# Kernel optimization log

Hardware: AMD Instinct MI355X
Metric: run time of the kernel (lower is better)

Reference implementation:

```python
import jax, jax.numpy as jnp
import numpy as np

NUM_GRAPHS = 1024


def _mlp2(h, Wa, ba, Wb, bb):
    # Linear -> ReLU -> Linear
    return jax.nn.relu(h @ Wa + ba) @ Wb + bb


def setup_inputs() -> dict:
    key = jax.random.key(0)
    ks = jax.random.split(key, 16)
    N, F, H, C, E = 100000, 128, 128, 10, 1600000
    x = jax.random.normal(ks[0], (N, F), dtype=jnp.float32)
    edge_index = jax.random.randint(ks[1], (2, E), 0, N, dtype=jnp.int64)
    batch = jnp.sort(jax.random.randint(ks[2], (N,), 0, NUM_GRAPHS, dtype=jnp.int64))
    s = 1.0 / np.sqrt(H)
    def w(k, shape):
        return jax.random.uniform(k, shape, jnp.float32, -s, s)
    return {
        "x": x, "edge_index": edge_index, "batch": batch,
        "W1a": w(ks[3], (F, H)), "b1a": w(ks[4], (H,)),
        "W1b": w(ks[5], (H, H)), "b1b": w(ks[6], (H,)),
        "W2a": w(ks[7], (H, H)), "b2a": w(ks[8], (H,)),
        "W2b": w(ks[9], (H, H)), "b2b": w(ks[10], (H,)),
        "Wl1": w(ks[11], (H, H)), "bl1": w(ks[12], (H,)),
        "Wl2": w(ks[13], (H, C)), "bl2": w(ks[14], (C,)),
    }


def reference(x, edge_index, batch, W1a, b1a, W1b, b1b, W2a, b2a, W2b, b2b, Wl1, bl1, Wl2, bl2):
    N = x.shape[0]
    src, dst = edge_index[0], edge_index[1]

    def gin_conv(h, Wa, ba, Wb, bb):
        # sum-aggregate neighbor features: agg[i] = sum_{(src->dst=i)} h[src]
        agg = jax.ops.segment_sum(h[src], dst, num_segments=N)
        # eps = 0 (PyG default): nn((1+eps)*h + agg)
        return _mlp2(h + agg, Wa, ba, Wb, bb)

    h = jax.nn.relu(gin_conv(x, W1a, b1a, W1b, b1b))
    h = jax.nn.relu(gin_conv(h, W2a, b2a, W2b, b2b))
    # global_add_pool over graph ids -> [num_graphs, H]
    g = jax.ops.segment_sum(h, batch, num_segments=NUM_GRAPHS)
    g = jax.nn.relu(g @ Wl1 + bl1)
    return jax.nn.log_softmax(g @ Wl2 + bl2, axis=1)
```

## Files before the change

kernel.cpp:

```cpp
#include <hip/hip_runtime.h>
#include <hip/hip_bf16.h>
#include <math.h>

#define NUM_GRAPHS 1024
#define SBLK 256
#define CAP 4096

typedef __attribute__((ext_vector_type(8))) short bf16x8;
typedef __attribute__((ext_vector_type(4))) float f32x4;

static __device__ __forceinline__ unsigned short f2bf(float f) {
    union { float f; unsigned u; } v; v.f = f;
    unsigned r = v.u + 0x7fffu + ((v.u >> 16) & 1u);
    return (unsigned short)(r >> 16);
}
static __device__ __forceinline__ float bf_lo(unsigned u) { return __uint_as_float(u << 16); }
static __device__ __forceinline__ float bf_hi(unsigned u) { return __uint_as_float(u & 0xffff0000u); }

static __device__ void scan_tot(const int* __restrict__ tot, int nbuck,
                                int* bb, int* tmp) {
    const int t = threadIdx.x;
    int v[4];
    int lsum = 0;
    #pragma unroll
    for (int j = 0; j < 4; ++j) {
        int idx = 4 * t + j;
        v[j] = (idx < nbuck) ? min(tot[idx], CAP) : 0;
        lsum += v[j];
    }
    tmp[t] = lsum;
    __syncthreads();
    for (int off = 1; off < 256; off <<= 1) {
        int a = (t >= off) ? tmp[t - off] : 0;
        __syncthreads();
        tmp[t] += a;
        __syncthreads();
    }
    int run = tmp[t] - lsum;
    #pragma unroll
    for (int j = 0; j < 4; ++j) {
        int idx = 4 * t + j;
        if (idx < nbuck) bb[idx] = run;
        run += v[j];
    }
    if (t == 255) bb[nbuck] = tmp[255];
    __syncthreads();
}

__global__ void k_sort(const int* __restrict__ eiSrc, const int* __restrict__ eiDst,
                       int E, int epb, int nbuck,
                       int* __restrict__ gcur, unsigned* __restrict__ ebuf,
                       const float* __restrict__ x, int N, unsigned* __restrict__ xb,
                       float* __restrict__ G,
                       const float* __restrict__ W0, const float* __restrict__ W1,
                       const float* __restrict__ W2, const float* __restrict__ W3,
                       unsigned short* __restrict__ wt) {
    if ((int)blockIdx.x < SBLK) {
        __shared__ int hist[1024];
        __shared__ int cur[1024];
        const int t = threadIdx.x;
        for (int i = t; i < 1024; i += 256) hist[i] = 0;
        __syncthreads();
        const int e0 = blockIdx.x * epb;
        const int e1 = min(E, e0 + epb);
        for (int e = e0 + t; e < e1; e += 256) atomicAdd(&hist[eiDst[e] >> 7], 1);
        __syncthreads();
        for (int b = t; b < nbuck; b += 256) {
            int c = hist[b];
            cur[b] = b * CAP + (c > 0 ? atomicAdd(&gcur[b], c) : 0);
        }
        __syncthreads();
        for (int e = e0 + t; e < e1; e += 256) {
            int d = eiDst[e];
            int s = eiSrc[e];
            int b = d >> 7;
            int pos = atomicAdd(&cur[b], 1);
            if (pos < (b + 1) * CAP)
                ebuf[pos] = (unsigned)s | ((unsigned)(d & 127) << 25);
        }
    } else if ((int)blockIdx.x < SBLK + 2048) {
        const int n4 = N * 32;
        int i = (blockIdx.x - SBLK) * 256 + threadIdx.x;
        const int stride = 2048 * 256;
        const float4* x4 = (const float4*)x;
        for (; i < n4; i += stride) {
            float4 v = x4[i];
            unsigned lo = (unsigned)f2bf(v.x) | ((unsigned)f2bf(v.y) << 16);
            unsigned hi = (unsigned)f2bf(v.z) | ((unsigned)f2bf(v.w) << 16);
            ((uint2*)xb)[i] = make_uint2(lo, hi);
        }
    } else if ((int)blockIdx.x < SBLK + 2048 + 64) {
        int i = (blockIdx.x - SBLK - 2048) * 256 + threadIdx.x;
        float4* G4 = (float4*)G;
        for (; i < NUM_GRAPHS * 32; i += 64 * 256)
            G4[i] = make_float4(0.f, 0.f, 0.f, 0.f);
    } else {
        int lb = blockIdx.x - SBLK - 2048 - 64;
        int b4 = lb >> 6;
        const float* W = (b4 == 0) ? W0 : (b4 == 1) ? W1 : (b4 == 2) ? W2 : W3;
        int idx = (lb & 63) * 256 + threadIdx.x;
        int k = idx >> 7, n = idx & 127;
        wt[b4 * 16384 + n * 128 + k] = f2bf(W[idx]);
    }
}

__global__ void k_bucket(const unsigned* __restrict__ ebuf, const int* __restrict__ gcur,
                         int nbuck, int N, int* __restrict__ rp, int* __restrict__ srcs) {
    __shared__ int bb[1025];
    __shared__ int tmp[256];
    __shared__ int h[128];
    __shared__ int cur[128];
    const int t = threadIdx.x;
    const int b = blockIdx.x;
    scan_tot(gcur, nbuck, bb, tmp);
    const int base = bb[b];
    const int cntb = bb[b + 1] - base;
    const unsigned* eb = ebuf + (size_t)b * CAP;
    if (t < 128) h[t] = 0;
    __syncthreads();
    for (int i = t; i < cntb; i += 256) atomicAdd(&h[eb[i] >> 25], 1);
    __syncthreads();
    int c0 = (t < 128) ? h[t] : 0;
    for (int off = 1; off < 128; off <<= 1) {
        int a = (t >= off && t < 128) ? h[t - off] : 0;
        __syncthreads();
        if (t < 128) h[t] += a;
        __syncthreads();
    }
    if (t < 128) {
        int excl = h[t] - c0;
        cur[t] = excl;
        int d = (b << 7) + t;
        if (d < N) rp[d] = base + excl;
        if (d == N) rp[N] = base + excl;
    }
    __syncthreads();
    for (int i = t; i < cntb; i += 256) {
        unsigned pck = eb[i];
        int pos = atomicAdd(&cur[pck >> 25], 1);
        srcs[base + pos] = (int)(pck & 0x01FFFFFFu);
    }
}

__device__ __forceinline__ void acc8(float* a, uint4 v) {
    a[0] += bf_lo(v.x); a[1] += bf_hi(v.x);
    a[2] += bf_lo(v.y); a[3] += bf_hi(v.y);
    a[4] += bf_lo(v.z); a[5] += bf_hi(v.z);
    a[6] += bf_lo(v.w); a[7] += bf_hi(v.w);
}

__global__ __launch_bounds__(256, 8)
void k_aggq(const uint4* __restrict__ H4, const int* __restrict__ rp,
            const int* __restrict__ srcs, int N, uint4* __restrict__ out) {
    int gw = (blockIdx.x * blockDim.x + threadIdx.x) >> 6;
    int lane = threadIdx.x & 63;
    int q = lane >> 4, ql = lane & 15;
    int n = gw * 4 + q;
    if (gw * 4 >= N) return;
    bool act = (n < N);
    int nc = act ? n : 0;
    uint4 s0 = H4[(size_t)nc * 16 + ql];
    float a[8];
    a[0] = bf_lo(s0.x); a[1] = bf_hi(s0.x);
    a[2] = bf_lo(s0.y); a[3] = bf_hi(s0.y);
    a[4] = bf_lo(s0.z); a[5] = bf_hi(s0.z);
    a[6] = bf_lo(s0.w); a[7] = bf_hi(s0.w);
    int j = act ? rp[nc] : 0;
    int e = act ? rp[nc + 1] : 0;
    while (j + 4 <= e) {
        int i0 = srcs[j], i1 = srcs[j + 1], i2 = srcs[j + 2], i3 = srcs[j + 3];
        uint4 v0 = H4[(size_t)i0 * 16 + ql];
        uint4 v1 = H4[(size_t)i1 * 16 + ql];
        uint4 v2 = H4[(size_t)i2 * 16 + ql];
        uint4 v3 = H4[(size_t)i3 * 16 + ql];
        acc8(a, v0); acc8(a, v1); acc8(a, v2); acc8(a, v3);
        j += 4;
    }
    while (j < e) {
        uint4 v = H4[(size_t)srcs[j] * 16 + ql];
        acc8(a, v);
        ++j;
    }
    if (act) {
        uint4 o;
        o.x = (unsigned)f2bf(a[0]) | ((unsigned)f2bf(a[1]) << 16);
        o.y = (unsigned)f2bf(a[2]) | ((unsigned)f2bf(a[3]) << 16);
        o.z = (unsigned)f2bf(a[4]) | ((unsigned)f2bf(a[5]) << 16);
        o.w = (unsigned)f2bf(a[6]) | ((unsigned)f2bf(a[7]) << 16);
        out[(size_t)n * 16 + ql] = o;
    }
}

__device__ __forceinline__ int swz_base(int row, int chunk) {
    return row * 128 + ((chunk ^ (row & 7)) << 3);
}

template <bool POOL>
__global__ __launch_bounds__(256, 2)
void k_mlp(const unsigned short* __restrict__ U, int N,
           const unsigned short* __restrict__ WaT, const float* __restrict__ ba,
           const unsigned short* __restrict__ WbT, const float* __restrict__ bb,
           unsigned short* __restrict__ Y,
           const int* __restrict__ batch, float* __restrict__ G) {
    __shared__ unsigned short lA[128 * 128];
    __shared__ unsigned short lW[128 * 128];
    __shared__ int bs[128];

    const int tid = threadIdx.x;
    const int lane = tid & 63;
    const int w = tid >> 6;
    const int wr = (w >> 1) * 64;
    const int wc = (w & 1) * 64;
    const int r0 = blockIdx.x * 128;

    {
        const uint4* U4 = (const uint4*)U;
        #pragma unroll
        for (int i = 0; i < 8; ++i) {
            int c = tid + 256 * i;
            int row = c >> 4, q = c & 15;
            uint4 v = (r0 + row < N) ? U4[(size_t)(r0 + row) * 16 + q]
                                     : make_uint4(0u, 0u, 0u, 0u);
            *(uint4*)&lA[swz_base(row, q)] = v;
        }
    }
    {
        const uint4* Wsrc = (const uint4*)WaT;
        #pragma unroll
        for (int i = 0; i < 8; ++i) {
            int c = tid + 256 * i;
            int row = c >> 4, q = c & 15;
            *(uint4*)&lW[swz_base(row, q)] = Wsrc[c];
        }
    }
    __syncthreads();

    const int am = lane & 15;
    const int kq = (lane >> 4) * 8;

    f32x4 acc[4][4];
    #pragma unroll
    for (int i = 0; i < 4; ++i)
        #pragma unroll
        for (int j = 0; j < 4; ++j) acc[i][j] = (f32x4){0.f, 0.f, 0.f, 0.f};

    #pragma unroll
    for (int ks = 0; ks < 4; ++ks) {
        int k0 = ks * 32 + kq;
        bf16x8 af[4], bq[4];
        #pragma unroll
        for (int i = 0; i < 4; ++i)
            af[i] = *(const bf16x8*)&lA[swz_base(wr + i * 16 + am, k0 >> 3)];
        #pragma unroll
        for (int j = 0; j < 4; ++j)
            bq[j] = *(const bf16x8*)&lW[swz_base(wc + j * 16 + am, k0 >> 3)];
        #pragma unroll
        for (int i = 0; i < 4; ++i)
            #pragma unroll
            for (int j = 0; j < 4; ++j)
                acc[i][j] = __builtin_amdgcn_mfma_f32_16x16x32_bf16(af[i], bq[j], acc[i][j], 0, 0, 0);
    }
    __syncthreads();

    #pragma unroll
    for (int j = 0; j < 4; ++j) {
        int col = wc + j * 16 + am;
        float bias = ba[col];
        #pragma unroll
        for (int i = 0; i < 4; ++i) {
            int rowb = wr + i * 16 + (lane >> 4) * 4;
            #pragma unroll
            for (int r = 0; r < 4; ++r) {
                float t = acc[i][j][r] + bias;
                t = t > 0.f ? t : 0.f;
                int row = rowb + r;
                lA[swz_base(row, col >> 3) + (col & 7)] = f2bf(t);
            }
        }
    }
    {
        const uint4* Wsrc = (const uint4*)WbT;
        #pragma unroll
        for (int i = 0; i < 8; ++i) {
            int c = tid + 256 * i;
            int row = c >> 4, q = c & 15;
            *(uint4*)&lW[swz_base(row, q)] = Wsrc[c];
        }
    }
    __syncthreads();

    #pragma unroll
    for (int i = 0; i < 4; ++i)
        #pragma unroll
        for (int j = 0; j < 4; ++j) acc[i][j] = (f32x4){0.f, 0.f, 0.f, 0.f};

    #pragma unroll
    for (int ks = 0; ks < 4; ++ks) {
        int k0 = ks * 32 + kq;
        bf16x8 af[4], bq[4];
        #pragma unroll
        for (int i = 0; i < 4; ++i)
            af[i] = *(const bf16x8*)&lA[swz_base(wr + i * 16 + am, k0 >> 3)];
        #pragma unroll
        for (int j = 0; j < 4; ++j)
            bq[j] = *(const bf16x8*)&lW[swz_base(wc + j * 16 + am, k0 >> 3)];
        #pragma unroll
        for (int i = 0; i < 4; ++i)
            #pragma unroll
            for (int j = 0; j < 4; ++j)
                acc[i][j] = __builtin_amdgcn_mfma_f32_16x16x32_bf16(af[i], bq[j], acc[i][j], 0, 0, 0);
    }

    if (!POOL) {
        #pragma unroll
        for (int j = 0; j < 4; ++j) {
            int col = wc + j * 16 + am;
            float bias = bb[col];
            #pragma unroll
            for (int i = 0; i < 4; ++i) {
                int rowb = wr + i * 16 + (lane >> 4) * 4;
                #pragma unroll
                for (int r = 0; r < 4; ++r) {
                    int row = r0 + rowb + r;
                    if (row < N) {
                        float t = acc[i][j][r] + bias;
                        t = t > 0.f ? t : 0.f;
                        Y[(size_t)row * 128 + col] = f2bf(t);
                    }
                }
            }
        }
    } else {
        __syncthreads();
        #pragma unroll
        for (int j = 0; j < 4; ++j) {
            int col = wc + j * 16 + am;
            float bias = bb[col];
            #pragma unroll
            for (int i = 0; i < 4; ++i) {
                int rowb = wr + i * 16 + (lane >> 4) * 4;
                #pragma unroll
                for (int r = 0; r < 4; ++r) {
                    float t = acc[i][j][r] + bias;
                    t = t > 0.f ? t : 0.f;
                    int row = rowb + r;
                    lA[swz_base(row, col >> 3) + (col & 7)] = f2bf(t);
                }
            }
        }
        if (tid < 128) bs[tid] = (r0 + tid < N) ? batch[r0 + tid] : -1;
        __syncthreads();
        const int col = tid & 127;
        const int half = tid >> 7;
        const int rbeg = half * 64, rend = rbeg + 64;
        float pacc = 0.f;
        int cur = bs[rbeg];
        for (int row = rbeg; row < rend; ++row) {
            int b = bs[row];
            if (b != cur) {
                if (cur >= 0) atomicAdd(&G[(size_t)cur * 128 + col], pacc);
                pacc = 0.f;
                cur = b;
            }
            unsigned short u = lA[swz_base(row, col >> 3) + (col & 7)];
            pacc += __uint_as_float((unsigned)u << 16);
        }
        if (cur >= 0) atomicAdd(&G[(size_t)cur * 128 + col], pacc);
    }
}

__global__ void k_head(const float* __restrict__ G,
                       const float* __restrict__ Wl1, const float* __restrict__ bl1,
                       const float* __restrict__ Wl2, const float* __restrict__ bl2,
                       int C, float* __restrict__ out) {
    __shared__ float sg[128];
    __shared__ float sh[128];
    __shared__ float sl[16];
    int row = blockIdx.x;
    int t = threadIdx.x;
    sg[t] = G[(size_t)row * 128 + t];
    __syncthreads();
    float a = bl1[t];
    for (int k = 0; k < 128; ++k) a += sg[k] * Wl1[k * 128 + t];
    sh[t] = a > 0.f ? a : 0.f;
    __syncthreads();
    if (t < C) {
        float l = bl2[t];
        for (int k = 0; k < 128; ++k) l += sh[k] * Wl2[k * C + t];
        sl[t] = l;
    }
    __syncthreads();
    if (t < C) {
        float m = -1e30f;
        for (int j = 0; j < C; ++j) m = fmaxf(m, sl[j]);
        float s = 0.f;
        for (int j = 0; j < C; ++j) s += __expf(sl[j] - m);
        out[(size_t)row * C + t] = sl[t] - m - __logf(s);
    }
}

extern "C" void kernel_launch(void* const* d_in, const int* in_sizes, int n_in,
                              void* d_out, int out_size, void* d_ws, size_t ws_size,
                              hipStream_t stream) {
    const float* x    = (const float*)d_in[0];
    const int*   ei   = (const int*)d_in[1];
    const int*   batch= (const int*)d_in[2];
    const float* W1a  = (const float*)d_in[3];
    const float* b1a  = (const float*)d_in[4];
    const float* W1b  = (const float*)d_in[5];
    const float* b1b  = (const float*)d_in[6];
    const float* W2a  = (const float*)d_in[7];
    const float* b2a  = (const float*)d_in[8];
    const float* W2b  = (const float*)d_in[9];
    const float* b2b  = (const float*)d_in[10];
    const float* Wl1  = (const float*)d_in[11];
    const float* bl1  = (const float*)d_in[12];
    const float* Wl2  = (const float*)d_in[13];
    const float* bl2  = (const float*)d_in[14];
    float* out = (float*)d_out;

    const int N = in_sizes[2];
    const int E = in_sizes[1] / 2;
    const int C = in_sizes[13] / 128;

    const int nbuck = (N >> 7) + 1;
    const int epb = (E + SBLK - 1) / SBLK;

    char* p = (char*)d_ws;
    auto alloc = [&](size_t bytes) {
        char* r = p;
        p += (bytes + 255) & ~(size_t)255;
        return r;
    };
    unsigned* xb   = (unsigned*)alloc((size_t)N * 64 * 4);
    unsigned* hA   = (unsigned*)alloc((size_t)N * 64 * 4);
    unsigned* hB   = (unsigned*)alloc((size_t)N * 64 * 4);
    float* g       = (float*)alloc((size_t)NUM_GRAPHS * 128 * 4);
    int* rp        = (int*)alloc((size_t)(N + 1) * 4);
    int* srcs      = (int*)alloc((size_t)E * 4);
    unsigned* ebuf = (unsigned*)alloc((size_t)nbuck * CAP * 4);
    int* gcur      = (int*)alloc((size_t)1024 * 4);
    unsigned short* wt = (unsigned short*)alloc((size_t)4 * 16384 * 2);
    (void)ws_size; (void)n_in; (void)out_size;

    hipMemsetAsync(gcur, 0, (size_t)nbuck * 4, stream);

    k_sort<<<SBLK + 2048 + 64 + 256, 256, 0, stream>>>(
        ei, ei + E, E, epb, nbuck, gcur, ebuf, x, N, xb, g,
        W1a, W1b, W2a, W2b, wt);
    k_bucket<<<nbuck, 256, 0, stream>>>(ebuf, gcur, nbuck, N, rp, srcs);

    const int mb = (N + 127) / 128;
    const int qw = (N + 3) / 4;
    const int qb = (qw + 3) / 4;

    k_aggq<<<qb, 256, 0, stream>>>((const uint4*)xb, rp, srcs, N, (uint4*)hA);
    k_mlp<false><<<mb, 256, 0, stream>>>((const unsigned short*)hA, N, wt, b1a,
                                         wt + 16384, b1b, (unsigned short*)hB,
                                         nullptr, nullptr);
    k_aggq<<<qb, 256, 0, stream>>>((const uint4*)hB, rp, srcs, N, (uint4*)hA);
    k_mlp<true><<<mb, 256, 0, stream>>>((const unsigned short*)hA, N, wt + 2 * 16384, b2a,
                                        wt + 3 * 16384, b2b, nullptr,
                                        batch, g);
    k_head<<<NUM_GRAPHS, 128, 0, stream>>>(g, Wl1, bl1, Wl2, bl2, C, out);
}
```

Before: 368.0 us.

## Fuse bucket CSR construction with first-layer neighbor aggregation

```diff
diff --git a/kernel.cpp b/kernel.cpp
--- a/kernel.cpp
+++ b/kernel.cpp
@@ -104,12 +104,16 @@
     }
 }
 
-__global__ void k_bucket(const unsigned* __restrict__ ebuf, const int* __restrict__ gcur,
-                         int nbuck, int N, int* __restrict__ rp, int* __restrict__ srcs) {
+__global__ __launch_bounds__(256, 6)
+void k_bktagg(const unsigned* __restrict__ ebuf, const int* __restrict__ gcur,
+              int nbuck, int N, int* __restrict__ rp, int* __restrict__ srcs,
+              const uint4* __restrict__ H4, uint4* __restrict__ out) {
     __shared__ int bb[1025];
     __shared__ int tmp[256];
     __shared__ int h[128];
     __shared__ int cur[128];
+    __shared__ int lrp[129];
+    __shared__ int lsrcs[CAP];
     const int t = threadIdx.x;
     const int b = blockIdx.x;
     scan_tot(gcur, nbuck, bb, tmp);
@@ -130,6 +134,8 @@
     if (t < 128) {
         int excl = h[t] - c0;
         cur[t] = excl;
+        lrp[t] = excl;
+        if (t == 127) lrp[128] = h[127];
         int d = (b << 7) + t;
         if (d < N) rp[d] = base + excl;
         if (d == N) rp[N] = base + excl;
@@ -138,7 +144,57 @@
     for (int i = t; i < cntb; i += 256) {
         unsigned pck = eb[i];
         int pos = atomicAdd(&cur[pck >> 25], 1);
-        srcs[base + pos] = (int)(pck & 0x01FFFFFFu);
+        int sv = (int)(pck & 0x01FFFFFFu);
+        lsrcs[pos] = sv;
+        srcs[base + pos] = sv;
+    }
+    __syncthreads();
+
+    const int lane = t & 63;
+    const int w = t >> 6;
+    const int q = lane >> 4, ql = lane & 15;
+    const int qid = w * 4 + q;
+    for (int nn = 0; nn < 8; ++nn) {
+        const int loc = qid * 8 + nn;
+        const int n = (b << 7) + loc;
+        if (n >= N) break;
+        uint4 s0 = H4[(size_t)n * 16 + ql];
+        float a[8];
+        a[0] = bf_lo(s0.x); a[1] = bf_hi(s0.x);
+        a[2] = bf_lo(s0.y); a[3] = bf_hi(s0.y);
+        a[4] = bf_lo(s0.z); a[5] = bf_hi(s0.z);
+        a[6] = bf_lo(s0.w); a[7] = bf_hi(s0.w);
+        int j = lrp[loc], e = lrp[loc + 1];
+        while (j + 4 <= e) {
+            int i0 = lsrcs[j], i1 = lsrcs[j + 1], i2 = lsrcs[j + 2], i3 = lsrcs[j + 3];
+            uint4 v0 = H4[(size_t)i0 * 16 + ql];
+            uint4 v1 = H4[(size_t)i1 * 16 + ql];
+            uint4 v2 = H4[(size_t)i2 * 16 + ql];
+            uint4 v3 = H4[(size_t)i3 * 16 + ql];
+            a[0] += bf_lo(v0.x) + bf_lo(v1.x) + bf_lo(v2.x) + bf_lo(v3.x);
+            a[1] += bf_hi(v0.x) + bf_hi(v1.x) + bf_hi(v2.x) + bf_hi(v3.x);
+            a[2] += bf_lo(v0.y) + bf_lo(v1.y) + bf_lo(v2.y) + bf_lo(v3.y);
+            a[3] += bf_hi(v0.y) + bf_hi(v1.y) + bf_hi(v2.y) + bf_hi(v3.y);
+            a[4] += bf_lo(v0.z) + bf_lo(v1.z) + bf_lo(v2.z) + bf_lo(v3.z);
+            a[5] += bf_hi(v0.z) + bf_hi(v1.z) + bf_hi(v2.z) + bf_hi(v3.z);
+            a[6] += bf_lo(v0.w) + bf_lo(v1.w) + bf_lo(v2.w) + bf_lo(v3.w);
+            a[7] += bf_hi(v0.w) + bf_hi(v1.w) + bf_hi(v2.w) + bf_hi(v3.w);
+            j += 4;
+        }
+        while (j < e) {
+            uint4 v = H4[(size_t)lsrcs[j] * 16 + ql];
+            a[0] += bf_lo(v.x); a[1] += bf_hi(v.x);
+            a[2] += bf_lo(v.y); a[3] += bf_hi(v.y);
+            a[4] += bf_lo(v.z); a[5] += bf_hi(v.z);
+            a[6] += bf_lo(v.w); a[7] += bf_hi(v.w);
+            ++j;
+        }
+        uint4 o;
+        o.x = (unsigned)f2bf(a[0]) | ((unsigned)f2bf(a[1]) << 16);
+        o.y = (unsigned)f2bf(a[2]) | ((unsigned)f2bf(a[3]) << 16);
+        o.z = (unsigned)f2bf(a[4]) | ((unsigned)f2bf(a[5]) << 16);
+        o.w = (unsigned)f2bf(a[6]) | ((unsigned)f2bf(a[7]) << 16);
+        out[(size_t)n * 16 + ql] = o;
     }
 }
 
@@ -448,13 +504,13 @@
     k_sort<<<SBLK + 2048 + 64 + 256, 256, 0, stream>>>(
         ei, ei + E, E, epb, nbuck, gcur, ebuf, x, N, xb, g,
         W1a, W1b, W2a, W2b, wt);
-    k_bucket<<<nbuck, 256, 0, stream>>>(ebuf, gcur, nbuck, N, rp, srcs);
 
     const int mb = (N + 127) / 128;
     const int qw = (N + 3) / 4;
     const int qb = (qw + 3) / 4;
 
-    k_aggq<<<qb, 256, 0, stream>>>((const uint4*)xb, rp, srcs, N, (uint4*)hA);
+    k_bktagg<<<nbuck, 256, 0, stream>>>(ebuf, gcur, nbuck, N, rp, srcs,
+                                        (const uint4*)xb, (uint4*)hA);
     k_mlp<false><<<mb, 256, 0, stream>>>((const unsigned short*)hA, N, wt, b1a,
                                          wt + 16384, b1b, (unsigned short*)hB,
                                          nullptr, nullptr);
```

Result: faster. 354.8 us (-3.6%).

## Fuse CSR bucketing, neighbor gather and MLP into per-layer conv kernels

Applied to the files above, without the earlier changes.

```diff
diff --git a/kernel.cpp b/kernel.cpp
--- a/kernel.cpp
+++ b/kernel.cpp
@@ -16,6 +16,10 @@
 }
 static __device__ __forceinline__ float bf_lo(unsigned u) { return __uint_as_float(u << 16); }
 static __device__ __forceinline__ float bf_hi(unsigned u) { return __uint_as_float(u & 0xffff0000u); }
+
+__device__ __forceinline__ int swz_base(int row, int chunk) {
+    return row * 128 + ((chunk ^ (row & 7)) << 3);
+}
 
 static __device__ void scan_tot(const int* __restrict__ tot, int nbuck,
                                 int* bb, int* tmp) {
@@ -104,126 +108,12 @@
     }
 }
 
-__global__ void k_bucket(const unsigned* __restrict__ ebuf, const int* __restrict__ gcur,
-                         int nbuck, int N, int* __restrict__ rp, int* __restrict__ srcs) {
-    __shared__ int bb[1025];
-    __shared__ int tmp[256];
-    __shared__ int h[128];
-    __shared__ int cur[128];
-    const int t = threadIdx.x;
-    const int b = blockIdx.x;
-    scan_tot(gcur, nbuck, bb, tmp);
-    const int base = bb[b];
-    const int cntb = bb[b + 1] - base;
-    const unsigned* eb = ebuf + (size_t)b * CAP;
-    if (t < 128) h[t] = 0;
-    __syncthreads();
-    for (int i = t; i < cntb; i += 256) atomicAdd(&h[eb[i] >> 25], 1);
-    __syncthreads();
-    int c0 = (t < 128) ? h[t] : 0;
-    for (int off = 1; off < 128; off <<= 1) {
-        int a = (t >= off && t < 128) ? h[t - off] : 0;
-        __syncthreads();
-        if (t < 128) h[t] += a;
-        __syncthreads();
-    }
-    if (t < 128) {
-        int excl = h[t] - c0;
-        cur[t] = excl;
-        int d = (b << 7) + t;
-        if (d < N) rp[d] = base + excl;
-        if (d == N) rp[N] = base + excl;
-    }
-    __syncthreads();
-    for (int i = t; i < cntb; i += 256) {
-        unsigned pck = eb[i];
-        int pos = atomicAdd(&cur[pck >> 25], 1);
-        srcs[base + pos] = (int)(pck & 0x01FFFFFFu);
-    }
-}
-
-__device__ __forceinline__ void acc8(float* a, uint4 v) {
-    a[0] += bf_lo(v.x); a[1] += bf_hi(v.x);
-    a[2] += bf_lo(v.y); a[3] += bf_hi(v.y);
-    a[4] += bf_lo(v.z); a[5] += bf_hi(v.z);
-    a[6] += bf_lo(v.w); a[7] += bf_hi(v.w);
-}
-
-__global__ __launch_bounds__(256, 8)
-void k_aggq(const uint4* __restrict__ H4, const int* __restrict__ rp,
-            const int* __restrict__ srcs, int N, uint4* __restrict__ out) {
-    int gw = (blockIdx.x * blockDim.x + threadIdx.x) >> 6;
-    int lane = threadIdx.x & 63;
-    int q = lane >> 4, ql = lane & 15;
-    int n = gw * 4 + q;
-    if (gw * 4 >= N) return;
-    bool act = (n < N);
-    int nc = act ? n : 0;
-    uint4 s0 = H4[(size_t)nc * 16 + ql];
-    float a[8];
-    a[0] = bf_lo(s0.x); a[1] = bf_hi(s0.x);
-    a[2] = bf_lo(s0.y); a[3] = bf_hi(s0.y);
-    a[4] = bf_lo(s0.z); a[5] = bf_hi(s0.z);
-    a[6] = bf_lo(s0.w); a[7] = bf_hi(s0.w);
-    int j = act ? rp[nc] : 0;
-    int e = act ? rp[nc + 1] : 0;
-    while (j + 4 <= e) {
-        int i0 = srcs[j], i1 = srcs[j + 1], i2 = srcs[j + 2], i3 = srcs[j + 3];
-        uint4 v0 = H4[(size_t)i0 * 16 + ql];
-        uint4 v1 = H4[(size_t)i1 * 16 + ql];
-        uint4 v2 = H4[(size_t)i2 * 16 + ql];
-        uint4 v3 = H4[(size_t)i3 * 16 + ql];
-        acc8(a, v0); acc8(a, v1); acc8(a, v2); acc8(a, v3);
-        j += 4;
-    }
-    while (j < e) {
-        uint4 v = H4[(size_t)srcs[j] * 16 + ql];
-        acc8(a, v);
-        ++j;
-    }
-    if (act) {
-        uint4 o;
-        o.x = (unsigned)f2bf(a[0]) | ((unsigned)f2bf(a[1]) << 16);
-        o.y = (unsigned)f2bf(a[2]) | ((unsigned)f2bf(a[3]) << 16);
-        o.z = (unsigned)f2bf(a[4]) | ((unsigned)f2bf(a[5]) << 16);
-        o.w = (unsigned)f2bf(a[6]) | ((unsigned)f2bf(a[7]) << 16);
-        out[(size_t)n * 16 + ql] = o;
-    }
-}
-
-__device__ __forceinline__ int swz_base(int row, int chunk) {
-    return row * 128 + ((chunk ^ (row & 7)) << 3);
-}
-
-template <bool POOL>
-__global__ __launch_bounds__(256, 2)
-void k_mlp(const unsigned short* __restrict__ U, int N,
-           const unsigned short* __restrict__ WaT, const float* __restrict__ ba,
-           const unsigned short* __restrict__ WbT, const float* __restrict__ bb,
-           unsigned short* __restrict__ Y,
-           const int* __restrict__ batch, float* __restrict__ G) {
-    __shared__ unsigned short lA[128 * 128];
-    __shared__ unsigned short lW[128 * 128];
-    __shared__ int bs[128];
-
-    const int tid = threadIdx.x;
-    const int lane = tid & 63;
-    const int w = tid >> 6;
-    const int wr = (w >> 1) * 64;
-    const int wc = (w & 1) * 64;
-    const int r0 = blockIdx.x * 128;
-
-    {
-        const uint4* U4 = (const uint4*)U;
-        #pragma unroll
-        for (int i = 0; i < 8; ++i) {
-            int c = tid + 256 * i;
-            int row = c >> 4, q = c & 15;
-            uint4 v = (r0 + row < N) ? U4[(size_t)(r0 + row) * 16 + q]
-                                     : make_uint4(0u, 0u, 0u, 0u);
-            *(uint4*)&lA[swz_base(row, q)] = v;
-        }
-    }
+__device__ __forceinline__ void mlp_core(unsigned short* lA, unsigned short* lW,
+                                         const unsigned short* __restrict__ WaT,
+                                         const float* __restrict__ ba,
+                                         const unsigned short* __restrict__ WbT,
+                                         f32x4 (&acc)[4][4],
+                                         int tid, int lane, int wr, int wc) {
     {
         const uint4* Wsrc = (const uint4*)WaT;
         #pragma unroll
@@ -238,7 +128,6 @@
     const int am = lane & 15;
     const int kq = (lane >> 4) * 8;
 
-    f32x4 acc[4][4];
     #pragma unroll
     for (int i = 0; i < 4; ++i)
         #pragma unroll
@@ -310,63 +199,224 @@
             for (int j = 0; j < 4; ++j)
                 acc[i][j] = __builtin_amdgcn_mfma_f32_16x16x32_bf16(af[i], bq[j], acc[i][j], 0, 0, 0);
     }
-
-    if (!POOL) {
-        #pragma unroll
-        for (int j = 0; j < 4; ++j) {
-            int col = wc + j * 16 + am;
-            float bias = bb[col];
+}
+
+__device__ __forceinline__ uint4 gather_row(const uint4* __restrict__ H4, int n, int ql,
+                                            const int* lrp, const int* lsrcs, int loc) {
+    uint4 s0 = H4[(size_t)n * 16 + ql];
+    float a[8];
+    a[0] = bf_lo(s0.x); a[1] = bf_hi(s0.x);
+    a[2] = bf_lo(s0.y); a[3] = bf_hi(s0.y);
+    a[4] = bf_lo(s0.z); a[5] = bf_hi(s0.z);
+    a[6] = bf_lo(s0.w); a[7] = bf_hi(s0.w);
+    int j = lrp[loc], e = lrp[loc + 1];
+    while (j + 4 <= e) {
+        int i0 = lsrcs[j], i1 = lsrcs[j + 1], i2 = lsrcs[j + 2], i3 = lsrcs[j + 3];
+        uint4 v0 = H4[(size_t)i0 * 16 + ql];
+        uint4 v1 = H4[(size_t)i1 * 16 + ql];
+        uint4 v2 = H4[(size_t)i2 * 16 + ql];
+        uint4 v3 = H4[(size_t)i3 * 16 + ql];
+        a[0] += bf_lo(v0.x) + bf_lo(v1.x) + bf_lo(v2.x) + bf_lo(v3.x);
+        a[1] += bf_hi(v0.x) + bf_hi(v1.x) + bf_hi(v2.x) + bf_hi(v3.x);
+        a[2] += bf_lo(v0.y) + bf_lo(v1.y) + bf_lo(v2.y) + bf_lo(v3.y);
+        a[3] += bf_hi(v0.y) + bf_hi(v1.y) + bf_hi(v2.y) + bf_hi(v3.y);
+        a[4] += bf_lo(v0.z) + bf_lo(v1.z) + bf_lo(v2.z) + bf_lo(v3.z);
+        a[5] += bf_hi(v0.z) + bf_hi(v1.z) + bf_hi(v2.z) + bf_hi(v3.z);
+        a[6] += bf_lo(v0.w) + bf_lo(v1.w) + bf_lo(v2.w) + bf_lo(v3.w);
+        a[7] += bf_hi(v0.w) + bf_hi(v1.w) + bf_hi(v2.w) + bf_hi(v3.w);
+        j += 4;
+    }
+    while (j < e) {
+        uint4 v = H4[(size_t)lsrcs[j] * 16 + ql];
+        a[0] += bf_lo(v.x); a[1] += bf_hi(v.x);
+        a[2] += bf_lo(v.y); a[3] += bf_hi(v.y);
+        a[4] += bf_lo(v.z); a[5] += bf_hi(v.z);
+        a[6] += bf_lo(v.w); a[7] += bf_hi(v.w);
+        ++j;
+    }
+    uint4 o;
+    o.x = (unsigned)f2bf(a[0]) | ((unsigned)f2bf(a[1]) << 16);
+    o.y = (unsigned)f2bf(a[2]) | ((unsigned)f2bf(a[3]) << 16);
+    o.z = (unsigned)f2bf(a[4]) | ((unsigned)f2bf(a[5]) << 16);
+    o.w = (unsigned)f2bf(a[6]) | ((unsigned)f2bf(a[7]) << 16);
+    return o;
+}
+
+__global__ __launch_bounds__(256, 2)
+void k_conv1(const unsigned* __restrict__ ebuf, const int* __restrict__ gcur,
+             int nbuck, int N, int* __restrict__ rp, int* __restrict__ srcs,
+             const uint4* __restrict__ X4,
+             const unsigned short* __restrict__ WaT, const float* __restrict__ ba,
+             const unsigned short* __restrict__ WbT, const float* __restrict__ bb,
+             unsigned short* __restrict__ Y) {
+    __shared__ unsigned short lA[128 * 128];
+    __shared__ __align__(16) unsigned char uraw[32 * 1024];
+    int* bbp   = (int*)(uraw);
+    int* tmpp  = (int*)(uraw + 4352);
+    int* hp    = (int*)(uraw + 5376);
+    int* curp  = (int*)(uraw + 5888);
+    int* lrp   = (int*)(uraw + 6400);
+    int* lsrcs = (int*)(uraw + 6928);
+    unsigned short* lW = (unsigned short*)uraw;
+
+    const int t = threadIdx.x;
+    const int b = blockIdx.x;
+
+    scan_tot(gcur, nbuck, bbp, tmpp);
+    const int base = bbp[b];
+    const int cntb = bbp[b + 1] - base;
+    const unsigned* eb = ebuf + (size_t)b * CAP;
+    if (t < 128) hp[t] = 0;
+    __syncthreads();
+    for (int i = t; i < cntb; i += 256) atomicAdd(&hp[eb[i] >> 25], 1);
+    __syncthreads();
+    int c0 = (t < 128) ? hp[t] : 0;
+    for (int off = 1; off < 128; off <<= 1) {
+        int a = (t >= off && t < 128) ? hp[t - off] : 0;
+        __syncthreads();
+        if (t < 128) hp[t] += a;
+        __syncthreads();
+    }
+    if (t < 128) {
+        int excl = hp[t] - c0;
+        curp[t] = excl;
+        lrp[t] = excl;
+        if (t == 127) lrp[128] = hp[127];
+        int d = (b << 7) + t;
+        if (d < N) rp[d] = base + excl;
+        if (d == N) rp[N] = base + excl;
+    }
+    __syncthreads();
+    for (int i = t; i < cntb; i += 256) {
+        unsigned pck = eb[i];
+        int pos = atomicAdd(&curp[pck >> 25], 1);
+        int sv = (int)(pck & 0x01FFFFFFu);
+        lsrcs[pos] = sv;
+        srcs[base + pos] = sv;
+    }
+    __syncthreads();
+
+    const int lane = t & 63;
+    const int w = t >> 6;
+    const int q = lane >> 4, ql = lane & 15;
+    const int qid = w * 4 + q;
+    for (int nn = 0; nn < 8; ++nn) {
+        const int loc = qid * 8 + nn;
+        const int n = (b << 7) + loc;
+        uint4 o = make_uint4(0u, 0u, 0u, 0u);
+        if (n < N) o = gather_row(X4, n, ql, lrp, lsrcs, loc);
+        *(uint4*)&lA[swz_base(loc, ql)] = o;
+    }
+    __syncthreads();
+
+    const int wr = (w >> 1) * 64;
+    const int wc = (w & 1) * 64;
+    f32x4 acc[4][4];
+    mlp_core(lA, lW, WaT, ba, WbT, acc, t, lane, wr, wc);
+
+    const int am = lane & 15;
+    #pragma unroll
+    for (int j = 0; j < 4; ++j) {
+        int col = wc + j * 16 + am;
+        float bias = bb[col];
+        #pragma unroll
+        for (int i = 0; i < 4; ++i) {
+            int rowb = wr + i * 16 + (lane >> 4) * 4;
             #pragma unroll
-            for (int i = 0; i < 4; ++i) {
-                int rowb = wr + i * 16 + (lane >> 4) * 4;
-                #pragma unroll
-                for (int r = 0; r < 4; ++r) {
-                    int row = r0 + rowb + r;
-                    if (row < N) {
-                        float t = acc[i][j][r] + bias;
-                        t = t > 0.f ? t : 0.f;
-                        Y[(size_t)row * 128 + col] = f2bf(t);
-                    }
+            for (int r = 0; r < 4; ++r) {
+                int row = (b << 7) + rowb + r;
+                if (row < N) {
+                    float v = acc[i][j][r] + bias;
+                    v = v > 0.f ? v : 0.f;
+                    Y[(size_t)row * 128 + col] = f2bf(v);
                 }
             }
         }
-    } else {
-        __syncthreads();
-        #pragma unroll
-        for (int j = 0; j < 4; ++j) {
-            int col = wc + j * 16 + am;
-            float bias = bb[col];
+    }
+}
+
+__global__ __launch_bounds__(256, 2)
+void k_conv2(const int* __restrict__ rp, const int* __restrict__ srcs, int nbuck, int N,
+             const uint4* __restrict__ H4,
+             const unsigned short* __restrict__ WaT, const float* __restrict__ ba,
+             const unsigned short* __restrict__ WbT, const float* __restrict__ bb,
+             const int* __restrict__ batch, float* __restrict__ G) {
+    __shared__ unsigned short lA[128 * 128];
+    __shared__ __align__(16) unsigned char uraw[32 * 1024];
+    __shared__ int bs[128];
+    int* lrp   = (int*)(uraw);
+    int* lsrcs = (int*)(uraw + 528);
+    unsigned short* lW = (unsigned short*)uraw;
+
+    const int t = threadIdx.x;
+    const int b = blockIdx.x;
+
+    if (t < 129) {
+        int gd = (b << 7) + t;
+        if (gd > N) gd = N;
+        lrp[t] = rp[gd];
+    }
+    __syncthreads();
+    const int base = lrp[0];
+    const int cntb = lrp[128] - base;
+    for (int i = t; i < cntb; i += 256) lsrcs[i] = srcs[base + i];
+    if (t < 129) lrp[t] -= base;
+    __syncthreads();
+
+    const int lane = t & 63;
+    const int w = t >> 6;
+    const int q = lane >> 4, ql = lane & 15;
+    const int qid = w * 4 + q;
+    for (int nn = 0; nn < 8; ++nn) {
+        const int loc = qid * 8 + nn;
+        const int n = (b << 7) + loc;
+        uint4 o = make_uint4(0u, 0u, 0u, 0u);
+        if (n < N) o = gather_row(H4, n, ql, lrp, lsrcs, loc);
+        *(uint4*)&lA[swz_base(loc, ql)] = o;
+    }
+    __syncthreads();
+
+    const int wr = (w >> 1) * 64;
+    const int wc = (w & 1) * 64;
+    f32x4 acc[4][4];
+    mlp_core(lA, lW, WaT, ba, WbT, acc, t, lane, wr, wc);
+
+    __syncthreads();
+    const int am = lane & 15;
+    #pragma unroll
+    for (int j = 0; j < 4; ++j) {
+        int col = wc + j * 16 + am;
+        float bias = bb[col];
+        #pragma unroll
+        for (int i = 0; i < 4; ++i) {
+            int rowb = wr + i * 16 + (lane >> 4) * 4;
             #pragma unroll
-            for (int i = 0; i < 4; ++i) {
-                int rowb = wr + i * 16 + (lane >> 4) * 4;
-                #pragma unroll
-                for (int r = 0; r < 4; ++r) {
-                    float t = acc[i][j][r] + bias;
-                    t = t > 0.f ? t : 0.f;
-                    int row = rowb + r;
-                    lA[swz_base(row, col >> 3) + (col & 7)] = f2bf(t);
-                }
+            for (int r = 0; r < 4; ++r) {
+                float v = acc[i][j][r] + bias;
+                v = v > 0.f ? v : 0.f;
+                int row = rowb + r;
+                lA[swz_base(row, col >> 3) + (col & 7)] = f2bf(v);
             }
         }
-        if (tid < 128) bs[tid] = (r0 + tid < N) ? batch[r0 + tid] : -1;
-        __syncthreads();
-        const int col = tid & 127;
-        const int half = tid >> 7;
-        const int rbeg = half * 64, rend = rbeg + 64;
-        float pacc = 0.f;
-        int cur = bs[rbeg];
-        for (int row = rbeg; row < rend; ++row) {
-            int b = bs[row];
-            if (b != cur) {
-                if (cur >= 0) atomicAdd(&G[(size_t)cur * 128 + col], pacc);
-                pacc = 0.f;
-                cur = b;
-            }
-            unsigned short u = lA[swz_base(row, col >> 3) + (col & 7)];
-            pacc += __uint_as_float((unsigned)u << 16);
-        }
-        if (cur >= 0) atomicAdd(&G[(size_t)cur * 128 + col], pacc);
-    }
+    }
+    if (t < 128) bs[t] = ((b << 7) + t < N) ? batch[(b << 7) + t] : -1;
+    __syncthreads();
+    const int col = t & 127;
+    const int half = t >> 7;
+    const int rbeg = half * 64, rend = rbeg + 64;
+    float pacc = 0.f;
+    int cur = bs[rbeg];
+    for (int row = rbeg; row < rend; ++row) {
+        int bg = bs[row];
+        if (bg != cur) {
+            if (cur >= 0) atomicAdd(&G[(size_t)cur * 128 + col], pacc);
+            pacc = 0.f;
+            cur = bg;
+        }
+        unsigned short u = lA[swz_base(row, col >> 3) + (col & 7)];
+        pacc += __uint_as_float((unsigned)u << 16);
+    }
+    if (cur >= 0) atomicAdd(&G[(size_t)cur * 128 + col], pacc);
 }
 
 __global__ void k_head(const float* __restrict__ G,
@@ -433,7 +483,6 @@
         return r;
     };
     unsigned* xb   = (unsigned*)alloc((size_t)N * 64 * 4);
-    unsigned* hA   = (unsigned*)alloc((size_t)N * 64 * 4);
     unsigned* hB   = (unsigned*)alloc((size_t)N * 64 * 4);
     float* g       = (float*)alloc((size_t)NUM_GRAPHS * 128 * 4);
     int* rp        = (int*)alloc((size_t)(N + 1) * 4);
@@ -448,19 +497,12 @@
     k_sort<<<SBLK + 2048 + 64 + 256, 256, 0, stream>>>(
         ei, ei + E, E, epb, nbuck, gcur, ebuf, x, N, xb, g,
         W1a, W1b, W2a, W2b, wt);
-    k_bucket<<<nbuck, 256, 0, stream>>>(ebuf, gcur, nbuck, N, rp, srcs);
-
-    const int mb = (N + 127) / 128;
-    const int qw = (N + 3) / 4;
-    const int qb = (qw + 3) / 4;
-
-    k_aggq<<<qb, 256, 0, stream>>>((const uint4*)xb, rp, srcs, N, (uint4*)hA);
-    k_mlp<false><<<mb, 256, 0, stream>>>((const unsigned short*)hA, N, wt, b1a,
-                                         wt + 16384, b1b, (unsigned short*)hB,
-                                         nullptr, nullptr);
-    k_aggq<<<qb, 256, 0, stream>>>((const uint4*)hB, rp, srcs, N, (uint4*)hA);
-    k_mlp<true><<<mb, 256, 0, stream>>>((const unsigned short*)hA, N, wt + 2 * 16384, b2a,
-                                        wt + 3 * 16384, b2b, nullptr,
-                                        batch, g);
+
+    k_conv1<<<nbuck, 256, 0, stream>>>(ebuf, gcur, nbuck, N, rp, srcs,
+                                       (const uint4*)xb, wt, b1a, wt + 16384, b1b,
+                                       (unsigned short*)hB);
+    k_conv2<<<nbuck, 256, 0, stream>>>(rp, srcs, nbuck, N,
+                                       (const uint4*)hB, wt + 2 * 16384, b2a,
+                                       wt + 3 * 16384, b2b, batch, g);
     k_head<<<NUM_GRAPHS, 128, 0, stream>>>(g, Wl1, bl1, Wl2, bl2, C, out);
 }
```

New measurement: 370.4 us. Within noise of the previous version (+0.6%).
